# Performance work log

Hardware: AMD Instinct MI355X
Metric: run time of the kernel (lower is better)

Reference implementation:

```python
import jax, jax.numpy as jnp
import numpy as np

EMBED = 512
H = 8
HD = EMBED // H           # 64
NUM_CLS = 4
WIN = 32                  # one-sided window radius
DIL = 1
WLEN = 2 * WIN + 1        # 65
CTX = NUM_CLS + WLEN      # 69
PATCH_LEN = 8192
B = 1
S = NUM_CLS + PATCH_LEN
THETA = 10000.0
COORD_HIGH = 100000.0
NEG = -1e30


def _rotate_half(x):
    # [..., x1, x2, ...] -> [..., -x2, x1, ...]
    x1 = x[..., 0::2]
    x2 = x[..., 1::2]
    return jnp.stack([-x2, x1], axis=-1).reshape(x.shape)


def _rope2d(x, coords):
    # x: (B,H,L,HD), coords: (B,L,2)
    half = HD // 2
    inv_freq = 1.0 / (THETA ** (jnp.arange(0, half, 2, dtype=jnp.float32) / half))  # (half//2,)
    xy = coords / COORD_HIGH
    fx = xy[..., 0][..., None] * inv_freq   # (B,L,half//2)
    fy = xy[..., 1][..., None] * inv_freq
    fx = jnp.repeat(fx, 2, axis=-1)         # (B,L,half)
    fy = jnp.repeat(fy, 2, axis=-1)
    freqs = jnp.concatenate([fx, fy], axis=-1)[:, None]  # (B,1,L,HD)
    return x * jnp.cos(freqs) + _rotate_half(x) * jnp.sin(freqs)


def setup_inputs() -> dict:
    key = jax.random.key(0)
    k1, k2, k3, k4, k5, k6 = jax.random.split(key, 6)
    x = jax.random.normal(k1, (B, S, EMBED), dtype=jnp.float32)
    coords = jax.random.uniform(k2, (B, PATCH_LEN, 2), dtype=jnp.float32) * COORD_HIGH
    sc = 1.0 / np.sqrt(EMBED)
    w_qkv = jax.random.normal(k3, (3 * EMBED, EMBED), dtype=jnp.float32) * sc
    b_qkv = jax.random.normal(k4, (3 * EMBED,), dtype=jnp.float32) * 0.02
    w_out = jax.random.normal(k5, (EMBED, EMBED), dtype=jnp.float32) * sc
    b_out = jax.random.normal(k6, (EMBED,), dtype=jnp.float32) * 0.02
    return {"x": x, "coords": coords, "w_qkv": w_qkv, "b_qkv": b_qkv,
            "w_out": w_out, "b_out": b_out}


def _forward(x, coords, w_qkv, b_qkv, w_out, b_out):
    Bb, seq_len, _ = x.shape
    qkv = x @ w_qkv.T + b_qkv                       # (B,S,3E)
    qkv = qkv.reshape(Bb, seq_len, 3, H, HD)
    qkv = jnp.transpose(qkv, (2, 0, 3, 1, 4))       # (3,B,H,S,HD)
    q, k, v = qkv[0], qkv[1], qkv[2]
    q_cls, k_cls, v_cls = q[:, :, :NUM_CLS], k[:, :, :NUM_CLS], v[:, :, :NUM_CLS]
    q_p, k_p, v_p = q[:, :, NUM_CLS:], k[:, :, NUM_CLS:], v[:, :, NUM_CLS:]

    q_p = _rope2d(q_p, coords)
    k_p = _rope2d(k_p, coords)
    k_all = jnp.concatenate([k_cls, k_p], axis=2)
    v_all = v

    scale = 1.0 / np.sqrt(HD)

    # --- global CLS attention: CLS queries attend to everything ---
    cls_scores = jnp.einsum('bhqd,bhkd->bhqk', q_cls, k_all) * scale
    cls_probs = jax.nn.softmax(cls_scores, axis=-1)
    cls_out = jnp.einsum('bhqk,bhkd->bhqd', cls_probs, v_all)

    # --- windowed patch attention: patch i -> [CLS | patches i-W..i+W (dilated)] ---
    L = PATCH_LEN
    pad = WIN * DIL
    k_pad = jnp.pad(k_p, ((0, 0), (0, 0), (pad, pad), (0, 0)))
    v_pad = jnp.pad(v_p, ((0, 0), (0, 0), (pad, pad), (0, 0)))
    gather_idx = jnp.arange(L)[:, None] + jnp.arange(WLEN)[None, :] * DIL  # (L,WLEN)
    k_win = k_pad[:, :, gather_idx]   # (B,H,L,WLEN,HD)
    v_win = v_pad[:, :, gather_idx]

    s_cls = jnp.einsum('bhld,bhcd->bhlc', q_p, k_cls) * scale     # (B,H,L,NUM_CLS)
    s_win = jnp.einsum('bhld,bhlwd->bhlw', q_p, k_win) * scale    # (B,H,L,WLEN)

    pos = jnp.arange(L)[:, None] + (jnp.arange(WLEN)[None, :] - WIN) * DIL
    in_bounds = (pos >= 0) & (pos < L)                            # (L,WLEN)
    s_win = jnp.where(in_bounds[None, None], s_win, NEG)

    scores = jnp.concatenate([s_cls, s_win], axis=-1)             # (B,H,L,CTX)
    probs = jax.nn.softmax(scores, axis=-1)
    p_cls, p_win = probs[..., :NUM_CLS], probs[..., NUM_CLS:]
    patch_out = (jnp.einsum('bhlc,bhcd->bhld', p_cls, v_cls)
                 + jnp.einsum('bhlw,bhlwd->bhld', p_win, v_win))

    out = jnp.concatenate([cls_out, patch_out], axis=2)           # (B,H,S,HD)
    out = jnp.transpose(out, (0, 2, 1, 3)).reshape(Bb, seq_len, EMBED)
    return out @ w_out.T + b_out


def reference(x, coords, w_qkv, b_qkv, w_out, b_out):
    return _forward(x, coords, w_qkv, b_qkv, w_out, b_out)
```

## Files before the change

kernel.cpp:

```cpp
#include <hip/hip_runtime.h>
#include <math.h>

#define EMBED 512
#define NHEAD 8
#define HD 64
#define NUM_CLS 4
#define WIN 32
#define WLEN 65
#define PATCH_LEN 8192
#define S_TOT 8196
#define QKV_LD 1536
#define VT_LD 8200

typedef short bf16x8 __attribute__((ext_vector_type(8)));
typedef float f32x4 __attribute__((ext_vector_type(4)));

__device__ __forceinline__ unsigned short f2bf(float f) {
    unsigned u = __float_as_uint(f);
    return (unsigned short)((u + 0x7fffu + ((u >> 16) & 1u)) >> 16);
}
__device__ __forceinline__ float bf2f(unsigned short v) {
    return __uint_as_float((unsigned)v << 16);
}
__device__ __forceinline__ void gll16(const unsigned short* g, unsigned short* l) {
    __builtin_amdgcn_global_load_lds((const __attribute__((address_space(1))) void*)g,
                                     (__attribute__((address_space(3))) void*)l, 16, 0, 0);
}
__device__ __forceinline__ bf16x8 pack8(float4 lo, float4 hi) {
    bf16x8 r;
    r[0] = (short)f2bf(lo.x); r[1] = (short)f2bf(lo.y);
    r[2] = (short)f2bf(lo.z); r[3] = (short)f2bf(lo.w);
    r[4] = (short)f2bf(hi.x); r[5] = (short)f2bf(hi.y);
    r[6] = (short)f2bf(hi.z); r[7] = (short)f2bf(hi.w);
    return r;
}

__global__ __launch_bounds__(256) void cast_w(const float* __restrict__ wq,
                                              const float* __restrict__ wo,
                                              unsigned short* __restrict__ wqb,
                                              unsigned short* __restrict__ wob)
{
    const int n2 = 3 * EMBED * EMBED;
    const int n3 = EMBED * EMBED;
    const int i = (blockIdx.x * 256 + threadIdx.x) * 4;
    const float* src;
    unsigned short* dst;
    int j;
    if (i < n2)           { src = wq; dst = wqb; j = i; }
    else if (i < n2 + n3) { src = wo; dst = wob; j = i - n2; }
    else return;
    const float4 v = *(const float4*)(src + j);
    ushort4 o;
    o.x = f2bf(v.x); o.y = f2bf(v.y); o.z = f2bf(v.z); o.w = f2bf(v.w);
    *(ushort4*)(dst + j) = o;
}

#define EXW 136
__global__ __launch_bounds__(256) void gemm_qkv(const float* __restrict__ X,
                                                const unsigned short* __restrict__ B,
                                                const float* __restrict__ bias,
                                                unsigned short* __restrict__ C,
                                                const float* __restrict__ coords,
                                                unsigned short* __restrict__ vT)
{
    const int M = S_TOT, N = 3 * EMBED, K = EMBED;
    __shared__ __align__(16) unsigned short SMEM[16384];
    unsigned short* EX = SMEM;

    const int tid = threadIdx.x;
    const int lane = tid & 63, w = tid >> 6;
    const int xcd = blockIdx.x & 7;
    const int s = blockIdx.x >> 3;
    const int bm = xcd + 8 * (s / 12);
    const int bn = s % 12;
    if (bm >= 65) return;

    const int ar0 = tid >> 2;
    const int col8 = (tid & 3) * 8;
    int gm0 = bm * 128 + ar0;       if (gm0 >= M) gm0 = M - 1;
    int gm1 = bm * 128 + ar0 + 64;  if (gm1 >= M) gm1 = M - 1;
    const float* Xp0 = X + (size_t)gm0 * K + col8;
    const float* Xp1 = X + (size_t)gm1 * K + col8;
    const unsigned short* pb0 = B + (size_t)(bn * 128 + ar0) * K + col8;
    const unsigned short* pb1 = B + (size_t)(bn * 128 + ar0 + 64) * K + col8;

    const int wr = (w & 1) * 64;
    const int wc = (w >> 1) * 64;
    const int fr = lane & 15;
    const int fk = (lane >> 4) * 8;

    f32x4 acc[4][4];
#pragma unroll
    for (int mi = 0; mi < 4; ++mi)
#pragma unroll
        for (int ni = 0; ni < 4; ++ni) acc[mi][ni] = (f32x4)0.f;

    {
        const float4 a00 = *(const float4*)(Xp0);
        const float4 a01 = *(const float4*)(Xp0 + 4);
        const float4 a10 = *(const float4*)(Xp1);
        const float4 a11 = *(const float4*)(Xp1 + 4);
        gll16(pb0, SMEM + 8192 + tid * 8);
        gll16(pb1, SMEM + 8192 + (tid + 256) * 8);
        *(bf16x8*)(SMEM + tid * 8) = pack8(a00, a01);
        *(bf16x8*)(SMEM + (tid + 256) * 8) = pack8(a10, a11);
    }

    for (int it = 0; it < 16; ++it) {
        __syncthreads();
        float4 n00, n01, n10, n11;
        const bool more = (it + 1 < 16);
        if (more) {
            const int kf = (it + 1) * 32;
            n00 = *(const float4*)(Xp0 + kf);
            n01 = *(const float4*)(Xp0 + kf + 4);
            n10 = *(const float4*)(Xp1 + kf);
            n11 = *(const float4*)(Xp1 + kf + 4);
            const int off = ((it + 1) & 1) * 4096;
            gll16(pb0 + kf, SMEM + 8192 + off + tid * 8);
            gll16(pb1 + kf, SMEM + 8192 + off + (tid + 256) * 8);
        }
        const unsigned short* Asb = SMEM + (it & 1) * 4096;
        const unsigned short* Bsb = SMEM + 8192 + (it & 1) * 4096;
        bf16x8 af[4], bf[4];
#pragma unroll
        for (int mi = 0; mi < 4; ++mi)
            af[mi] = *(const bf16x8*)(Asb + (wr + mi * 16 + fr) * 32 + fk);
#pragma unroll
        for (int ni = 0; ni < 4; ++ni)
            bf[ni] = *(const bf16x8*)(Bsb + (wc + ni * 16 + fr) * 32 + fk);
#pragma unroll
        for (int mi = 0; mi < 4; ++mi)
#pragma unroll
            for (int ni = 0; ni < 4; ++ni)
                acc[mi][ni] = __builtin_amdgcn_mfma_f32_16x16x32_bf16(af[mi], bf[ni], acc[mi][ni], 0, 0, 0);
        if (more) {
            const int off = ((it + 1) & 1) * 4096;
            *(bf16x8*)(SMEM + off + tid * 8) = pack8(n00, n01);
            *(bf16x8*)(SMEM + off + (tid + 256) * 8) = pack8(n10, n11);
        }
    }
    __syncthreads();

    const int ccol = bn * 128 + wc + fr;

    if (bn < 8) {
        ushort2* rt = (ushort2*)EX;
        for (int idx = tid; idx < 4096; idx += 256) {
            const int rr = idx >> 5, pr = idx & 31;
            int l = bm * 128 + rr - NUM_CLS;
            l = l < 0 ? 0 : (l > PATCH_LEN - 1 ? PATCH_LEN - 1 : l);
            const float cxy = coords[l * 2 + (pr >> 4)] * 1e-5f;
            const float f = cxy * __expf(-(float)(pr & 15) * 0.5756462732485114f);
            float sn, cs;
            __sincosf(f, &sn, &cs);
            ushort2 e; e.x = f2bf(cs); e.y = f2bf(sn);
            rt[idx] = e;
        }
        __syncthreads();

        unsigned pv[4][4][2];
#pragma unroll
        for (int mi = 0; mi < 4; ++mi) {
#pragma unroll
            for (int r = 0; r < 4; ++r) {
                const int rloc = wr + mi * 16 + (lane >> 4) * 4 + r;
                const int row = bm * 128 + rloc;
                const bool patch = (row >= NUM_CLS) && (row < M);
#pragma unroll
                for (int ni = 0; ni < 4; ++ni) {
                    const int col = ccol + ni * 16;
                    const float biased = acc[mi][ni][r] + bias[col];
                    const float prt = __shfl_xor(biased, 1);
                    float outv = biased;
                    if (patch) {
                        const ushort2 e = rt[rloc * 32 + ((col & 63) >> 1)];
                        const float cs = bf2f(e.x), sn = bf2f(e.y);
                        outv = (col & 1) ? (biased * cs + prt * sn)
                                         : (biased * cs - prt * sn);
                    }
                    const unsigned us = f2bf(outv);
                    if (r & 1) pv[mi][ni][r >> 1] |= us << 16;
                    else       pv[mi][ni][r >> 1] = us;
                }
            }
        }
        for (int p = 0; p < 2; ++p) {
            __syncthreads();
            if ((w & 1) == p) {
#pragma unroll
                for (int mi = 0; mi < 4; ++mi) {
#pragma unroll
                    for (int r = 0; r < 4; ++r) {
                        const int rl = mi * 16 + (lane >> 4) * 4 + r;
#pragma unroll
                        for (int ni = 0; ni < 4; ++ni) {
                            const unsigned pw = pv[mi][ni][r >> 1];
                            EX[rl * EXW + wc + fr + ni * 16] =
                                (unsigned short)((r & 1) ? (pw >> 16) : (pw & 0xffff));
                        }
                    }
                }
            }
            __syncthreads();
#pragma unroll
            for (int i = 0; i < 4; ++i) {
                const int idx = tid + 256 * i;
                const int rowl = idx >> 4, ch = idx & 15;
                const int grow = bm * 128 + p * 64 + rowl;
                if (grow < M)
                    *(bf16x8*)(C + (size_t)grow * N + bn * 128 + ch * 8) =
                        *(const bf16x8*)(EX + rowl * EXW + ch * 8);
            }
        }
    } else {
        const int dbase = (bn - 8) * 128;
#pragma unroll
        for (int mi = 0; mi < 4; ++mi) {
            const int rbase = bm * 128 + wr + mi * 16 + (lane >> 4) * 4;
#pragma unroll
            for (int ni = 0; ni < 4; ++ni) {
                const int col = ccol + ni * 16;
#pragma unroll
                for (int r = 0; r < 4; ++r) {
                    const int row = rbase + r;
                    if (row < M)
                        C[(size_t)row * N + col] = f2bf(acc[mi][ni][r] + bias[col]);
                }
            }
        }
        for (int p = 0; p < 2; ++p) {
            __syncthreads();
            if ((w >> 1) == p) {
#pragma unroll
                for (int mi = 0; mi < 4; ++mi) {
                    const int tok0 = wr + mi * 16 + (lane >> 4) * 4;
                    const int rw = bm * 128 + tok0;
#pragma unroll
                    for (int ni = 0; ni < 4; ++ni) {
                        const int col = ccol + ni * 16;
                        const int dloc = fr + 16 * ni;
                        ushort4 o;
                        o.x = (rw + 0 < M) ? f2bf(acc[mi][ni][0] + bias[col]) : (unsigned short)0;
                        o.y = (rw + 1 < M) ? f2bf(acc[mi][ni][1] + bias[col]) : (unsigned short)0;
                        o.z = (rw + 2 < M) ? f2bf(acc[mi][ni][2] + bias[col]) : (unsigned short)0;
                        o.w = (rw + 3 < M) ? f2bf(acc[mi][ni][3] + bias[col]) : (unsigned short)0;
                        *(ushort4*)(EX + dloc * EXW + tok0) = o;
                    }
                }
            }
            __syncthreads();
            const int d = tid >> 2;
            const int tch = (tid & 3) * 32;
            const int gtok = bm * 128 + tch;
            unsigned short* dst = vT + (size_t)(dbase + p * 64 + d) * VT_LD + gtok;
            const unsigned short* srcl = EX + d * EXW + tch;
            if (gtok + 32 <= VT_LD) {
#pragma unroll
                for (int c2 = 0; c2 < 32; c2 += 8)
                    *(bf16x8*)(dst + c2) = *(const bf16x8*)(srcl + c2);
            } else {
                for (int c2 = 0; c2 < 32; ++c2)
                    if (gtok + c2 < VT_LD) dst[c2] = srcl[c2];
            }
        }
    }
}

__global__ __launch_bounds__(256) void gemm_out(const unsigned short* __restrict__ A,
                                                const unsigned short* __restrict__ B,
                                                const float* __restrict__ bias,
                                                float* __restrict__ C)
{
    const int M = S_TOT, N = EMBED, K = EMBED;
    __shared__ __align__(16) unsigned short As[2][64 * 32];
    __shared__ __align__(16) unsigned short Bs[2][128 * 32];
    const int tid = threadIdx.x;
    const int lane = tid & 63, w = tid >> 6;
    const int bn = blockIdx.x, bm = blockIdx.y;

    const int ar0 = tid >> 2;
    const int col8 = (tid & 3) * 8;
    int gm0 = bm * 64 + ar0;  if (gm0 >= M) gm0 = M - 1;
    const unsigned short* pa0 = A + (size_t)gm0 * K + col8;
    const unsigned short* pb0 = B + (size_t)(bn * 128 + ar0) * K + col8;
    const unsigned short* pb1 = B + (size_t)(bn * 128 + ar0 + 64) * K + col8;

    const int wr = (w & 1) * 32;
    const int wc = (w >> 1) * 64;
    const int fr = lane & 15;
    const int fk = (lane >> 4) * 8;

    f32x4 acc[2][4];
#pragma unroll
    for (int mi = 0; mi < 2; ++mi)
#pragma unroll
        for (int ni = 0; ni < 4; ++ni) acc[mi][ni] = (f32x4)0.f;

    gll16(pa0, As[0] + tid * 8);
    gll16(pb0, Bs[0] + tid * 8);
    gll16(pb1, Bs[0] + (tid + 256) * 8);

    for (int it = 0; it < 16; ++it) {
        __syncthreads();
        if (it + 1 < 16) {
            const int k0 = (it + 1) * 32;
            const int nb = (it + 1) & 1;
            gll16(pa0 + k0, As[nb] + tid * 8);
            gll16(pb0 + k0, Bs[nb] + tid * 8);
            gll16(pb1 + k0, Bs[nb] + (tid + 256) * 8);
        }
        const int cb = it & 1;
        bf16x8 af[2], bf[4];
#pragma unroll
        for (int mi = 0; mi < 2; ++mi)
            af[mi] = *(const bf16x8*)(As[cb] + (wr + mi * 16 + fr) * 32 + fk);
#pragma unroll
        for (int ni = 0; ni < 4; ++ni)
            bf[ni] = *(const bf16x8*)(Bs[cb] + (wc + ni * 16 + fr) * 32 + fk);
#pragma unroll
        for (int mi = 0; mi < 2; ++mi)
#pragma unroll
            for (int ni = 0; ni < 4; ++ni)
                acc[mi][ni] = __builtin_amdgcn_mfma_f32_16x16x32_bf16(af[mi], bf[ni], acc[mi][ni], 0, 0, 0);
    }

    const int ccol = bn * 128 + wc + fr;
#pragma unroll
    for (int mi = 0; mi < 2; ++mi) {
        const int rbase = bm * 64 + wr + mi * 16 + (lane >> 4) * 4;
#pragma unroll
        for (int r = 0; r < 4; ++r) {
            const int row = rbase + r;
            if (row < M) {
#pragma unroll
                for (int ni = 0; ni < 4; ++ni)
                    C[(size_t)row * N + ccol + ni * 16] = acc[mi][ni][r] + bias[ccol + ni * 16];
            }
        }
    }
}

#define CCH 128
#define NCHUNK ((S_TOT + CCH - 1) / CCH)
#define PSTRIDE 68
#define SW 116
#define PW 136

__global__ __launch_bounds__(256) void attn_fused(
    const unsigned short* __restrict__ qkv,
    const unsigned short* __restrict__ vT,
    float* __restrict__ part,
    unsigned short* __restrict__ attnb)
{
    __shared__ __align__(16) char SM[49664];
    const int tid = threadIdx.x;
    const int lane = tid & 63, w = tid >> 6;

    if (blockIdx.x < 2048) {
        const int l0 = (blockIdx.x >> 3) * 32;
        const int h = blockIdx.x & 7;
        unsigned short* Qs = (unsigned short*)SM;
        unsigned short* Ks = (unsigned short*)(SM + 4096);
        unsigned short* Vt = (unsigned short*)(SM + 18432);
        float* Sm = (float*)(SM + 34816);

        {
            const int i = tid;
            const int t = i >> 3;
            const int dcl = (i & 7) ^ (t & 7);
            gll16(qkv + (size_t)(NUM_CLS + l0 + t) * QKV_LD + h * HD + dcl * 8, Qs + i * 8);
        }
        for (int i = tid; i < 896; i += 256) {
            const int c = i >> 3;
            const int dcl = (i & 7) ^ (c & 7);
            int tok = (c >= 104 && c < 108) ? (c - 104) : (l0 - 32 + c);
            tok = tok < 0 ? 0 : (tok > S_TOT - 1 ? S_TOT - 1 : tok);
            gll16(qkv + (size_t)tok * QKV_LD + EMBED + h * HD + dcl * 8, Ks + i * 8);
        }
        for (int i = tid; i < 1024; i += 256) {
            const int d = i >> 4;
            const int kcl = (i & 15) ^ (d & 15);
            const int c0 = kcl * 8;
            int tokb = (c0 == 104) ? 0 : (l0 - 32 + c0);
            tokb = tokb < 0 ? 0 : (tokb > 8192 ? 8192 : tokb);
            gll16(vT + (size_t)(h * HD + d) * VT_LD + tokb, Vt + i * 8);
        }
        __syncthreads();

        bf16x8 qf[2][2];
#pragma unroll
        for (int mt = 0; mt < 2; ++mt)
#pragma unroll
            for (int ks = 0; ks < 2; ++ks) {
                const int row = mt * 16 + (lane & 15);
                const int dc = (ks * 4 + (lane >> 4)) ^ (row & 7);
                qf[mt][ks] = *(const bf16x8*)(Qs + row * 64 + dc * 8);
            }
        for (int idx = w; idx < 14; idx += 4) {
            const int mt = idx & 1, nt = idx >> 1;
            f32x4 acc = (f32x4)0.f;
#pragma unroll
            for (int ks = 0; ks < 2; ++ks) {
                const int kr = nt * 16 + (lane & 15);
                const int dc = (ks * 4 + (lane >> 4)) ^ (kr & 7);
                const bf16x8 kf = *(const bf16x8*)(Ks + kr * 64 + dc * 8);
                acc = __builtin_amdgcn_mfma_f32_16x16x32_bf16(qf[mt][ks], kf, acc, 0, 0, 0);
            }
            const int col = nt * 16 + (lane & 15);
            const int r0 = mt * 16 + (lane >> 4) * 4;
#pragma unroll
            for (int r = 0; r < 4; ++r) Sm[(r0 + r) * SW + col] = acc[r];
        }
        __syncthreads();

        {
            const int t = tid >> 3, lq = tid & 7;
            float e[14];
            float m = -INFINITY;
#pragma unroll
            for (int j = 0; j < 14; ++j) {
                const int c = lq + 8 * j;
                bool valid;
                if (c >= 104) valid = (c < 108);
                else {
                    const int r = c - 4;
                    const int pos = l0 - 32 + r;
                    valid = (c >= 4) && (c < 100) && (r >= t) && (r <= t + 64) &&
                            (pos >= 0) && (pos < PATCH_LEN);
                }
                e[j] = valid ? Sm[t * SW + c] * 0.125f : -INFINITY;
                m = fmaxf(m, e[j]);
            }
#pragma unroll
            for (int off = 1; off < 8; off <<= 1) m = fmaxf(m, __shfl_xor(m, off, 64));
            float sum = 0.f;
#pragma unroll
            for (int j = 0; j < 14; ++j) { e[j] = expf(e[j] - m); sum += e[j]; }
#pragma unroll
            for (int off = 1; off < 8; off <<= 1) sum += __shfl_xor(sum, off, 64);
            const float inv = 1.f / sum;
            __syncthreads();
            unsigned short* P = (unsigned short*)Sm;
#pragma unroll
            for (int j = 0; j < 14; ++j) P[t * PW + lq + 8 * j] = f2bf(e[j] * inv);
            ushort2 z; z.x = 0; z.y = 0;
            *(ushort2*)(P + (tid >> 3) * PW + 112 + (tid & 7) * 2) = z;
        }
        __syncthreads();

        {
            const unsigned short* P = (const unsigned short*)Sm;
            const int mt = w & 1;
            bf16x8 pf[4];
#pragma unroll
            for (int ks = 0; ks < 4; ++ks) {
                const int row = mt * 16 + (lane & 15);
                pf[ks] = *(const bf16x8*)(P + row * PW + ks * 32 + (lane >> 4) * 8);
            }
#pragma unroll
            for (int nn = 0; nn < 2; ++nn) {
                const int nt = (w >> 1) + nn * 2;
                f32x4 acc = (f32x4)0.f;
#pragma unroll
                for (int ks = 0; ks < 4; ++ks) {
                    const int d = nt * 16 + (lane & 15);
                    const int kc = (ks * 4 + (lane >> 4)) ^ (d & 15);
                    const bf16x8 vf = *(const bf16x8*)(Vt + d * 128 + kc * 8);
                    acc = __builtin_amdgcn_mfma_f32_16x16x32_bf16(pf[ks], vf, acc, 0, 0, 0);
                }
                const int dcol = nt * 16 + (lane & 15);
                const int r0 = mt * 16 + (lane >> 4) * 4;
#pragma unroll
                for (int r = 0; r < 4; ++r)
                    attnb[(size_t)(NUM_CLS + l0 + r0 + r) * EMBED + h * HD + dcol] = f2bf(acc[r]);
            }
        }
    } else {
        const int cid = blockIdx.x - 2048;
        const int h = cid & 7;
        const int c = cid >> 3;
        const int base = c * CCH;
        float* qs = (float*)SM;
        unsigned short* Kl = (unsigned short*)(SM + 1024);
        float* sc = (float*)(SM + 17408);
        float* ored = (float*)(SM + 19456);
        float* ml = (float*)(SM + 23552);

        {
            const int qi = tid >> 6, d = tid & 63;
            qs[qi * 64 + d] = bf2f(qkv[(size_t)qi * QKV_LD + h * HD + d]);
        }
        for (int i = tid; i < 1024; i += 256) {
            const int kr = i >> 3;
            const int dc = (i & 7) ^ (kr & 7);
            int j = base + kr; if (j > S_TOT - 1) j = S_TOT - 1;
            gll16(qkv + (size_t)j * QKV_LD + EMBED + h * HD + dc * 8, Kl + i * 8);
        }
        __syncthreads();

        {
            const int jj = tid & 127;
            const int qp = (tid >> 7) * 2;
            const int j = base + jj;
            float s0 = -INFINITY, s1 = -INFINITY;
            if (j < S_TOT) {
                float a0 = 0.f, a1 = 0.f;
#pragma unroll
                for (int cch = 0; cch < 8; ++cch) {
                    const int slot = cch ^ (jj & 7);
                    const bf16x8 kv8 = *(const bf16x8*)(Kl + jj * 64 + slot * 8);
#pragma unroll
                    for (int u = 0; u < 8; ++u) {
                        const float kf = bf2f((unsigned short)kv8[u]);
                        a0 += qs[(qp + 0) * 64 + cch * 8 + u] * kf;
                        a1 += qs[(qp + 1) * 64 + cch * 8 + u] * kf;
                    }
                }
                s0 = a0 * 0.125f; s1 = a1 * 0.125f;
            }
            sc[(qp + 0) * CCH + jj] = s0;
            sc[(qp + 1) * CCH + jj] = s1;
        }
        __syncthreads();

        {
            float m = fmaxf(sc[w * CCH + lane], sc[w * CCH + lane + 64]);
#pragma unroll
            for (int off = 32; off > 0; off >>= 1) m = fmaxf(m, __shfl_xor(m, off, 64));
            const float e0 = expf(sc[w * CCH + lane] - m);
            const float e1 = expf(sc[w * CCH + lane + 64] - m);
            sc[w * CCH + lane] = e0; sc[w * CCH + lane + 64] = e1;
            float lsum = e0 + e1;
#pragma unroll
            for (int off = 32; off > 0; off >>= 1) lsum += __shfl_xor(lsum, off, 64);
            if (lane == 0) { ml[w * 2 + 0] = m; ml[w * 2 + 1] = lsum; }
        }
        __syncthreads();

        {
            const int g = w, d = lane;
            float a0 = 0.f, a1 = 0.f, a2 = 0.f, a3 = 0.f;
            for (int jj = g; jj < CCH; jj += 4) {
                const int j = base + jj;
                if (j >= S_TOT) break;
                const float vv = bf2f(qkv[(size_t)j * QKV_LD + 2 * EMBED + h * HD + d]);
                a0 += sc[0 * CCH + jj] * vv; a1 += sc[1 * CCH + jj] * vv;
                a2 += sc[2 * CCH + jj] * vv; a3 += sc[3 * CCH + jj] * vv;
            }
            ored[(g * 4 + 0) * 64 + d] = a0; ored[(g * 4 + 1) * 64 + d] = a1;
            ored[(g * 4 + 2) * 64 + d] = a2; ored[(g * 4 + 3) * 64 + d] = a3;
        }
        __syncthreads();

        {
            const int qi = tid >> 6, d = tid & 63;
            const float o = ored[(0 * 4 + qi) * 64 + d] + ored[(1 * 4 + qi) * 64 + d] +
                            ored[(2 * 4 + qi) * 64 + d] + ored[(3 * 4 + qi) * 64 + d];
            float* pb = part + ((size_t)(h * NCHUNK + c) * 4 + qi) * PSTRIDE;
            pb[d] = o;
            if (d == 0) { pb[64] = ml[qi * 2 + 0]; pb[65] = ml[qi * 2 + 1]; }
        }
    }
}

__global__ __launch_bounds__(256) void cls_attn_combine(const float* __restrict__ part,
                                                        unsigned short* __restrict__ attn)
{
    const int h = blockIdx.x;
    const int qi = threadIdx.x >> 6, d = threadIdx.x & 63;
    float M = -INFINITY;
    for (int c = 0; c < NCHUNK; ++c)
        M = fmaxf(M, part[((size_t)(h * NCHUNK + c) * 4 + qi) * PSTRIDE + 64]);
    float acc = 0.f, L = 0.f;
    for (int c = 0; c < NCHUNK; ++c) {
        const float* pb = part + ((size_t)(h * NCHUNK + c) * 4 + qi) * PSTRIDE;
        const float s = expf(pb[64] - M);
        acc += s * pb[d];
        L   += s * pb[65];
    }
    attn[(size_t)qi * EMBED + h * HD + d] = f2bf(acc / L);
}

extern "C" void kernel_launch(void* const* d_in, const int* in_sizes, int n_in,
                              void* d_out, int out_size, void* d_ws, size_t ws_size,
                              hipStream_t stream)
{
    const float* x      = (const float*)d_in[0];
    const float* coords = (const float*)d_in[1];
    const float* w_qkv  = (const float*)d_in[2];
    const float* b_qkv  = (const float*)d_in[3];
    const float* w_out  = (const float*)d_in[4];
    const float* b_out  = (const float*)d_in[5];
    float* out = (float*)d_out;

    char* p = (char*)d_ws;
    unsigned short* qkv   = (unsigned short*)p;  p += (size_t)S_TOT * QKV_LD * 2;
    unsigned short* vT    = (unsigned short*)p;  p += (size_t)EMBED * VT_LD * 2;
    unsigned short* attnb = (unsigned short*)p;  p += (size_t)S_TOT * EMBED * 2;
    float*          part  = (float*)p;           p += (size_t)NHEAD * NCHUNK * 4 * PSTRIDE * 4;
    unsigned short* wob   = (unsigned short*)p;  p += (size_t)EMBED * EMBED * 2;
    unsigned short* wqb   = (unsigned short*)p;


    cast_w<<<1024, 256, 0, stream>>>(w_qkv, w_out, wqb, wob);

    gemm_qkv<<<864, 256, 0, stream>>>(x, wqb, b_qkv, qkv, coords, vT);

    attn_fused<<<2048 + NHEAD * NCHUNK, 256, 0, stream>>>(qkv, vT, part, attnb);

    cls_attn_combine<<<NHEAD, 256, 0, stream>>>(part, attnb);

    gemm_out<<<dim3(4, 129), 256, 0, stream>>>(attnb, wob, b_out, out);
}
```

Before: 178.6 us.

## Triple-buffer GEMM K-loops, swizzle LDS tiles, precompute RoPE table in cast kernel

Both GEMMs move from double to triple-buffered LDS staging. They use explicit vmcnt waits and raw barriers so global loads run two stages ahead of the MFMA work. LDS row chunks get an XOR swizzle to cut bank conflicts on fragment reads. The RoPE cos/sin table is now computed once in the weight-cast kernel and streamed into LDS with global_load_lds, instead of being recomputed per block with sincos. The extra LDS per block and the launch_bounds occupancy hint may lower occupancy.

```diff
diff --git a/kernel.cpp b/kernel.cpp
--- a/kernel.cpp
+++ b/kernel.cpp
@@ -37,34 +37,47 @@
 
 __global__ __launch_bounds__(256) void cast_w(const float* __restrict__ wq,
                                               const float* __restrict__ wo,
+                                              const float* __restrict__ coords,
                                               unsigned short* __restrict__ wqb,
-                                              unsigned short* __restrict__ wob)
+                                              unsigned short* __restrict__ wob,
+                                              ushort2* __restrict__ rt)
 {
-    const int n2 = 3 * EMBED * EMBED;
-    const int n3 = EMBED * EMBED;
-    const int i = (blockIdx.x * 256 + threadIdx.x) * 4;
-    const float* src;
-    unsigned short* dst;
-    int j;
-    if (i < n2)           { src = wq; dst = wqb; j = i; }
-    else if (i < n2 + n3) { src = wo; dst = wob; j = i - n2; }
-    else return;
-    const float4 v = *(const float4*)(src + j);
-    ushort4 o;
-    o.x = f2bf(v.x); o.y = f2bf(v.y); o.z = f2bf(v.z); o.w = f2bf(v.w);
-    *(ushort4*)(dst + j) = o;
+    if (blockIdx.x < 1024) {
+        const int n2 = 3 * EMBED * EMBED;
+        const int n3 = EMBED * EMBED;
+        const int i = (blockIdx.x * 256 + threadIdx.x) * 4;
+        const float* src;
+        unsigned short* dst;
+        int j;
+        if (i < n2)           { src = wq; dst = wqb; j = i; }
+        else if (i < n2 + n3) { src = wo; dst = wob; j = i - n2; }
+        else return;
+        const float4 v = *(const float4*)(src + j);
+        ushort4 o;
+        o.x = f2bf(v.x); o.y = f2bf(v.y); o.z = f2bf(v.z); o.w = f2bf(v.w);
+        *(ushort4*)(dst + j) = o;
+    } else {
+        const int idx = (blockIdx.x - 1024) * 256 + threadIdx.x;
+        const int l = idx >> 5, pr = idx & 31;
+        const float cxy = coords[l * 2 + (pr >> 4)] * 1e-5f;
+        const float f = cxy * __expf(-(float)(pr & 15) * 0.5756462732485114f);
+        float sn, cs;
+        __sincosf(f, &sn, &cs);
+        ushort2 e; e.x = f2bf(cs); e.y = f2bf(sn);
+        rt[idx] = e;
+    }
 }
 
 #define EXW 136
-__global__ __launch_bounds__(256) void gemm_qkv(const float* __restrict__ X,
-                                                const unsigned short* __restrict__ B,
-                                                const float* __restrict__ bias,
-                                                unsigned short* __restrict__ C,
-                                                const float* __restrict__ coords,
-                                                unsigned short* __restrict__ vT)
+__global__ __launch_bounds__(256, 3) void gemm_qkv(const float* __restrict__ X,
+                                                   const unsigned short* __restrict__ B,
+                                                   const float* __restrict__ bias,
+                                                   unsigned short* __restrict__ C,
+                                                   const ushort2* __restrict__ RT,
+                                                   unsigned short* __restrict__ vT)
 {
     const int M = S_TOT, N = 3 * EMBED, K = EMBED;
-    __shared__ __align__(16) unsigned short SMEM[16384];
+    __shared__ __align__(16) unsigned short SMEM[24576];
     unsigned short* EX = SMEM;
 
     const int tid = threadIdx.x;
@@ -76,18 +89,18 @@
     if (bm >= 65) return;
 
     const int ar0 = tid >> 2;
-    const int col8 = (tid & 3) * 8;
+    const int colsw = ((tid & 3) ^ ((tid >> 3) & 3)) * 8;
     int gm0 = bm * 128 + ar0;       if (gm0 >= M) gm0 = M - 1;
     int gm1 = bm * 128 + ar0 + 64;  if (gm1 >= M) gm1 = M - 1;
-    const float* Xp0 = X + (size_t)gm0 * K + col8;
-    const float* Xp1 = X + (size_t)gm1 * K + col8;
-    const unsigned short* pb0 = B + (size_t)(bn * 128 + ar0) * K + col8;
-    const unsigned short* pb1 = B + (size_t)(bn * 128 + ar0 + 64) * K + col8;
+    const float* Xp0 = X + (size_t)gm0 * K + colsw;
+    const float* Xp1 = X + (size_t)gm1 * K + colsw;
+    const unsigned short* pb0 = B + (size_t)(bn * 128 + ar0) * K + colsw;
+    const unsigned short* pb1 = B + (size_t)(bn * 128 + ar0 + 64) * K + colsw;
 
     const int wr = (w & 1) * 64;
     const int wc = (w >> 1) * 64;
     const int fr = lane & 15;
-    const int fk = (lane >> 4) * 8;
+    const int fkswz = (((lane >> 4) ^ ((fr >> 1) & 3))) * 8;
 
     f32x4 acc[4][4];
 #pragma unroll
@@ -95,67 +108,85 @@
 #pragma unroll
         for (int ni = 0; ni < 4; ++ni) acc[mi][ni] = (f32x4)0.f;
 
+    unsigned short* A0 = SMEM;
+    unsigned short* A1 = SMEM + 4096;
+    unsigned short* A2 = SMEM + 8192;
+    unsigned short* Bb0 = SMEM + 12288;
+    unsigned short* Bb1 = SMEM + 16384;
+    unsigned short* Bb2 = SMEM + 20480;
+
+    float4 n00, n01, n10, n11;
     {
         const float4 a00 = *(const float4*)(Xp0);
         const float4 a01 = *(const float4*)(Xp0 + 4);
         const float4 a10 = *(const float4*)(Xp1);
         const float4 a11 = *(const float4*)(Xp1 + 4);
-        gll16(pb0, SMEM + 8192 + tid * 8);
-        gll16(pb1, SMEM + 8192 + (tid + 256) * 8);
-        *(bf16x8*)(SMEM + tid * 8) = pack8(a00, a01);
-        *(bf16x8*)(SMEM + (tid + 256) * 8) = pack8(a10, a11);
+        gll16(pb0, Bb0 + tid * 8);
+        gll16(pb1, Bb0 + (tid + 256) * 8);
+        *(bf16x8*)(A0 + tid * 8) = pack8(a00, a01);
+        *(bf16x8*)(A0 + (tid + 256) * 8) = pack8(a10, a11);
+        asm volatile("" ::: "memory");
+        n00 = *(const float4*)(Xp0 + 32);
+        n01 = *(const float4*)(Xp0 + 36);
+        n10 = *(const float4*)(Xp1 + 32);
+        n11 = *(const float4*)(Xp1 + 36);
+        gll16(pb0 + 32, Bb1 + tid * 8);
+        gll16(pb1 + 32, Bb1 + (tid + 256) * 8);
     }
 
     for (int it = 0; it < 16; ++it) {
-        __syncthreads();
-        float4 n00, n01, n10, n11;
-        const bool more = (it + 1 < 16);
-        if (more) {
-            const int kf = (it + 1) * 32;
-            n00 = *(const float4*)(Xp0 + kf);
-            n01 = *(const float4*)(Xp0 + kf + 4);
-            n10 = *(const float4*)(Xp1 + kf);
-            n11 = *(const float4*)(Xp1 + kf + 4);
-            const int off = ((it + 1) & 1) * 4096;
-            gll16(pb0 + kf, SMEM + 8192 + off + tid * 8);
-            gll16(pb1 + kf, SMEM + 8192 + off + (tid + 256) * 8);
-        }
-        const unsigned short* Asb = SMEM + (it & 1) * 4096;
-        const unsigned short* Bsb = SMEM + 8192 + (it & 1) * 4096;
-        bf16x8 af[4], bf[4];
+        if (it < 15) asm volatile("s_waitcnt vmcnt(6) lgkmcnt(0)" ::: "memory");
+        else         asm volatile("s_waitcnt vmcnt(0) lgkmcnt(0)" ::: "memory");
+        __builtin_amdgcn_s_barrier();
+
+        float4 m00, m01, m10, m11;
+        const bool pf = (it < 14);
+        if (pf) {
+            const int kf = (it + 2) * 32;
+            m00 = *(const float4*)(Xp0 + kf);
+            m01 = *(const float4*)(Xp0 + kf + 4);
+            m10 = *(const float4*)(Xp1 + kf);
+            m11 = *(const float4*)(Xp1 + kf + 4);
+            gll16(pb0 + kf, Bb2 + tid * 8);
+            gll16(pb1 + kf, Bb2 + (tid + 256) * 8);
+        }
+
+        bf16x8 af[4], bfr[4];
 #pragma unroll
         for (int mi = 0; mi < 4; ++mi)
-            af[mi] = *(const bf16x8*)(Asb + (wr + mi * 16 + fr) * 32 + fk);
+            af[mi] = *(const bf16x8*)(A0 + (wr + mi * 16 + fr) * 32 + fkswz);
 #pragma unroll
         for (int ni = 0; ni < 4; ++ni)
-            bf[ni] = *(const bf16x8*)(Bsb + (wc + ni * 16 + fr) * 32 + fk);
+            bfr[ni] = *(const bf16x8*)(Bb0 + (wc + ni * 16 + fr) * 32 + fkswz);
 #pragma unroll
         for (int mi = 0; mi < 4; ++mi)
 #pragma unroll
             for (int ni = 0; ni < 4; ++ni)
-                acc[mi][ni] = __builtin_amdgcn_mfma_f32_16x16x32_bf16(af[mi], bf[ni], acc[mi][ni], 0, 0, 0);
-        if (more) {
-            const int off = ((it + 1) & 1) * 4096;
-            *(bf16x8*)(SMEM + off + tid * 8) = pack8(n00, n01);
-            *(bf16x8*)(SMEM + off + (tid + 256) * 8) = pack8(n10, n11);
-        }
+                acc[mi][ni] = __builtin_amdgcn_mfma_f32_16x16x32_bf16(af[mi], bfr[ni], acc[mi][ni], 0, 0, 0);
+
+        if (it < 15) {
+            *(bf16x8*)(A1 + tid * 8) = pack8(n00, n01);
+            *(bf16x8*)(A1 + (tid + 256) * 8) = pack8(n10, n11);
+        }
+        if (pf) { n00 = m00; n01 = m01; n10 = m10; n11 = m11; }
+
+        unsigned short* t;
+        t = A0;  A0 = A1;  A1 = A2;  A2 = t;
+        t = Bb0; Bb0 = Bb1; Bb1 = Bb2; Bb2 = t;
     }
     __syncthreads();
 
     const int ccol = bn * 128 + wc + fr;
 
     if (bn < 8) {
-        ushort2* rt = (ushort2*)EX;
-        for (int idx = tid; idx < 4096; idx += 256) {
-            const int rr = idx >> 5, pr = idx & 31;
-            int l = bm * 128 + rr - NUM_CLS;
+        const ushort2* rt = (const ushort2*)EX;
+#pragma unroll
+        for (int i0 = 0; i0 < 4; ++i0) {
+            const int i = tid + 256 * i0;
+            const int rloc = i >> 3, ch = i & 7;
+            int l = bm * 128 + rloc - NUM_CLS;
             l = l < 0 ? 0 : (l > PATCH_LEN - 1 ? PATCH_LEN - 1 : l);
-            const float cxy = coords[l * 2 + (pr >> 4)] * 1e-5f;
-            const float f = cxy * __expf(-(float)(pr & 15) * 0.5756462732485114f);
-            float sn, cs;
-            __sincosf(f, &sn, &cs);
-            ushort2 e; e.x = f2bf(cs); e.y = f2bf(sn);
-            rt[idx] = e;
+            gll16((const unsigned short*)(RT + (size_t)l * 32 + ch * 4), EX + i * 8);
         }
         __syncthreads();
 
@@ -273,23 +304,23 @@
                                                 float* __restrict__ C)
 {
     const int M = S_TOT, N = EMBED, K = EMBED;
-    __shared__ __align__(16) unsigned short As[2][64 * 32];
-    __shared__ __align__(16) unsigned short Bs[2][128 * 32];
+    __shared__ __align__(16) unsigned short AS[3][64 * 32];
+    __shared__ __align__(16) unsigned short BS[3][128 * 32];
     const int tid = threadIdx.x;
     const int lane = tid & 63, w = tid >> 6;
     const int bn = blockIdx.x, bm = blockIdx.y;
 
     const int ar0 = tid >> 2;
-    const int col8 = (tid & 3) * 8;
+    const int colsw = ((tid & 3) ^ ((tid >> 3) & 3)) * 8;
     int gm0 = bm * 64 + ar0;  if (gm0 >= M) gm0 = M - 1;
-    const unsigned short* pa0 = A + (size_t)gm0 * K + col8;
-    const unsigned short* pb0 = B + (size_t)(bn * 128 + ar0) * K + col8;
-    const unsigned short* pb1 = B + (size_t)(bn * 128 + ar0 + 64) * K + col8;
+    const unsigned short* pa0 = A + (size_t)gm0 * K + colsw;
+    const unsigned short* pb0 = B + (size_t)(bn * 128 + ar0) * K + colsw;
+    const unsigned short* pb1 = B + (size_t)(bn * 128 + ar0 + 64) * K + colsw;
 
     const int wr = (w & 1) * 32;
     const int wc = (w >> 1) * 64;
     const int fr = lane & 15;
-    const int fk = (lane >> 4) * 8;
+    const int fkswz = (((lane >> 4) ^ ((fr >> 1) & 3))) * 8;
 
     f32x4 acc[2][4];
 #pragma unroll
@@ -297,32 +328,42 @@
 #pragma unroll
         for (int ni = 0; ni < 4; ++ni) acc[mi][ni] = (f32x4)0.f;
 
-    gll16(pa0, As[0] + tid * 8);
-    gll16(pb0, Bs[0] + tid * 8);
-    gll16(pb1, Bs[0] + (tid + 256) * 8);
+    unsigned short *As0 = AS[0], *As1 = AS[1], *As2 = AS[2];
+    unsigned short *Bs0 = BS[0], *Bs1 = BS[1], *Bs2 = BS[2];
+
+    gll16(pa0, As0 + tid * 8);
+    gll16(pb0, Bs0 + tid * 8);
+    gll16(pb1, Bs0 + (tid + 256) * 8);
+    asm volatile("" ::: "memory");
+    gll16(pa0 + 32, As1 + tid * 8);
+    gll16(pb0 + 32, Bs1 + tid * 8);
+    gll16(pb1 + 32, Bs1 + (tid + 256) * 8);
 
     for (int it = 0; it < 16; ++it) {
-        __syncthreads();
-        if (it + 1 < 16) {
-            const int k0 = (it + 1) * 32;
-            const int nb = (it + 1) & 1;
-            gll16(pa0 + k0, As[nb] + tid * 8);
-            gll16(pb0 + k0, Bs[nb] + tid * 8);
-            gll16(pb1 + k0, Bs[nb] + (tid + 256) * 8);
-        }
-        const int cb = it & 1;
-        bf16x8 af[2], bf[4];
+        if (it < 15) asm volatile("s_waitcnt vmcnt(3)" ::: "memory");
+        else         asm volatile("s_waitcnt vmcnt(0)" ::: "memory");
+        __builtin_amdgcn_s_barrier();
+        if (it < 14) {
+            const int k0 = (it + 2) * 32;
+            gll16(pa0 + k0, As2 + tid * 8);
+            gll16(pb0 + k0, Bs2 + tid * 8);
+            gll16(pb1 + k0, Bs2 + (tid + 256) * 8);
+        }
+        bf16x8 af[2], bfr[4];
 #pragma unroll
         for (int mi = 0; mi < 2; ++mi)
-            af[mi] = *(const bf16x8*)(As[cb] + (wr + mi * 16 + fr) * 32 + fk);
+            af[mi] = *(const bf16x8*)(As0 + (wr + mi * 16 + fr) * 32 + fkswz);
 #pragma unroll
         for (int ni = 0; ni < 4; ++ni)
-            bf[ni] = *(const bf16x8*)(Bs[cb] + (wc + ni * 16 + fr) * 32 + fk);
+            bfr[ni] = *(const bf16x8*)(Bs0 + (wc + ni * 16 + fr) * 32 + fkswz);
 #pragma unroll
         for (int mi = 0; mi < 2; ++mi)
 #pragma unroll
             for (int ni = 0; ni < 4; ++ni)
-                acc[mi][ni] = __builtin_amdgcn_mfma_f32_16x16x32_bf16(af[mi], bf[ni], acc[mi][ni], 0, 0, 0);
+                acc[mi][ni] = __builtin_amdgcn_mfma_f32_16x16x32_bf16(af[mi], bfr[ni], acc[mi][ni], 0, 0, 0);
+        unsigned short* t;
+        t = As0; As0 = As1; As1 = As2; As2 = t;
+        t = Bs0; Bs0 = Bs1; Bs1 = Bs2; Bs2 = t;
     }
 
     const int ccol = bn * 128 + wc + fr;
@@ -600,12 +641,13 @@
     unsigned short* attnb = (unsigned short*)p;  p += (size_t)S_TOT * EMBED * 2;
     float*          part  = (float*)p;           p += (size_t)NHEAD * NCHUNK * 4 * PSTRIDE * 4;
     unsigned short* wob   = (unsigned short*)p;  p += (size_t)EMBED * EMBED * 2;
-    unsigned short* wqb   = (unsigned short*)p;
-
-
-    cast_w<<<1024, 256, 0, stream>>>(w_qkv, w_out, wqb, wob);
-
-    gemm_qkv<<<864, 256, 0, stream>>>(x, wqb, b_qkv, qkv, coords, vT);
+    unsigned short* wqb   = (unsigned short*)p;  p += (size_t)3 * EMBED * EMBED * 2;
+    ushort2*        ropet = (ushort2*)p;
+
+
+    cast_w<<<2048, 256, 0, stream>>>(w_qkv, w_out, coords, wqb, wob, ropet);
+
+    gemm_qkv<<<864, 256, 0, stream>>>(x, wqb, b_qkv, qkv, ropet, vT);
 
     attn_fused<<<2048 + NHEAD * NCHUNK, 256, 0, stream>>>(qkv, vT, part, attnb);
 
```

Measured after the change: 176.4 us. About the same (-1.2%).
